# Kernel optimization log

Hardware: AMD Instinct MI355X
Metric: run time of the kernel (lower is better)

## Reference

```python
import jax, jax.numpy as jnp
import numpy as np

HEADS = 2
BN_EPS = 1e-5


def _axial_self_attn(x, Wq, Wkv, Wout, bout):
    # x: (b, s, t, c) -- attend along t (the axial sequence dim)
    b, s, t, c = x.shape
    dh = c // HEADS
    q = (x @ Wq).reshape(b, s, t, HEADS, dh)
    k, v = jnp.split(x @ Wkv, 2, axis=-1)  # matches torch .chunk(2, dim=-1)
    k = k.reshape(b, s, t, HEADS, dh)
    v = v.reshape(b, s, t, HEADS, dh)
    dots = jnp.einsum('bsind,bsjnd->bsnij', q, k) * (dh ** -0.5)
    attn = jax.nn.softmax(dots, axis=-1)
    out = jnp.einsum('bsnij,bsjnd->bsind', attn, v).reshape(b, s, t, c)
    return out @ Wout + bout


def setup_inputs() -> dict:
    key = jax.random.key(0)
    ks = jax.random.split(key, 8)
    B, C, H, W = 8, 128, 256, 256
    E = 2 * C
    sd = 0.05
    return {
        'x': jax.random.normal(ks[0], (B, C, H, W), jnp.float32),
        'Wq_h': jax.random.normal(ks[1], (C, C), jnp.float32) * sd,
        'Wkv_h': jax.random.normal(ks[2], (C, 2 * C), jnp.float32) * sd,
        'Wout_h': jax.random.normal(ks[3], (C, C), jnp.float32) * sd,
        'bout_h': jnp.zeros((C,), jnp.float32),
        'Wq_w': jax.random.normal(ks[4], (C, C), jnp.float32) * sd,
        'Wkv_w': jax.random.normal(ks[5], (C, 2 * C), jnp.float32) * sd,
        'Wout_w': jax.random.normal(ks[6], (C, C), jnp.float32) * sd,
        'bout_w': jnp.zeros((C,), jnp.float32),
        'conv_w': jax.random.normal(ks[7], (E, E), jnp.float32) * sd,  # (in, out); torch conv weight[o,i,0,0].T
        'gamma': jnp.ones((E,), jnp.float32),
        'beta': jnp.zeros((E,), jnp.float32),
    }


def reference(x, Wq_h, Wkv_h, Wout_h, bout_h, Wq_w, Wkv_w, Wout_w, bout_w, conv_w, gamma, beta):
    B, C, H, W = x.shape
    # MaxPool2d(2)
    xp = x.reshape(B, C, H // 2, 2, W // 2, 2).max(axis=(3, 5))  # (B,C,H2,W2)
    xc = jnp.transpose(xp, (0, 2, 3, 1))  # (B,H2,W2,C) channels-last
    # AxialAttention, sum_axial_out=True: height-axis attn + width-axis attn
    a_h = _axial_self_attn(jnp.transpose(xc, (0, 2, 1, 3)), Wq_h, Wkv_h, Wout_h, bout_h)
    a_h = jnp.transpose(a_h, (0, 2, 1, 3))
    a_w = _axial_self_attn(xc, Wq_w, Wkv_w, Wout_w, bout_w)
    a = jax.nn.relu(a_h + a_w)
    # cat((x_attn, x), dim=channel) then conv1x1 -> relu -> BatchNorm (batch stats)
    y = jnp.concatenate([a, xc], axis=-1) @ conv_w  # (B,H2,W2,2C)
    y = jax.nn.relu(y)
    mean = y.mean(axis=(0, 1, 2))
    var = y.var(axis=(0, 1, 2))
    y = (y - mean) * jax.lax.rsqrt(var + BN_EPS) * gamma + beta
    return jnp.transpose(y, (0, 3, 1, 2))  # back to NCHW
```

## Files before the change

### kernel.cpp

```cpp
#include <hip/hip_runtime.h>


typedef short v8s __attribute__((ext_vector_type(8)));
typedef short v4s __attribute__((ext_vector_type(4)));
typedef float v4f __attribute__((ext_vector_type(4)));
typedef float v4flt __attribute__((ext_vector_type(4)));

#define LSA 136
#define LSC 264
#define LSP 130

static __device__ __forceinline__ short f2bf(float f){
  unsigned u = __builtin_bit_cast(unsigned, f);
  u = (u + 0x7FFFu + ((u >> 16) & 1u)) >> 16;
  return (short)u;
}
static __device__ __forceinline__ float bf2f(short s){
  unsigned u = ((unsigned)(unsigned short)s) << 16;
  return __builtin_bit_cast(float, u);
}

__global__ void prep_kernel(const float* __restrict__ Wq_h, const float* __restrict__ Wkv_h,
                            const float* __restrict__ Wout_h, const float* __restrict__ Wq_w,
                            const float* __restrict__ Wkv_w, const float* __restrict__ Wout_w,
                            const float* __restrict__ conv_w, short* __restrict__ wt,
                            float* __restrict__ stats){
  int idx = blockIdx.x * 256 + threadIdx.x;
  if (idx < 8192) stats[idx] = 0.0f;
  const float* src; int K, O, base;
  if      (idx <  16384){ base = 0;      K=128; O=128; src=Wq_h;  }
  else if (idx <  49152){ base = 16384;  K=128; O=256; src=Wkv_h; }
  else if (idx <  65536){ base = 49152;  K=128; O=128; src=Wout_h;}
  else if (idx <  81920){ base = 65536;  K=128; O=128; src=Wq_w;  }
  else if (idx < 114688){ base = 81920;  K=128; O=256; src=Wkv_w; }
  else if (idx < 131072){ base = 114688; K=128; O=128; src=Wout_w;}
  else                  { base = 131072; K=256; O=256; src=conv_w;}
  int local = idx - base;
  int o = local / K, i = local - o * K;
  wt[idx] = f2bf(src[i * O + o]);
}

__global__ __launch_bounds__(256, 4)
void pool_kernel(const float* __restrict__ x, short* __restrict__ xph,
                 short* __restrict__ xpw){
  __shared__ short t_[128*LSP];
  int bx = blockIdx.x;
  int b = bx >> 7, i = bx & 127;
  int tid = (int)threadIdx.x;
  int j2 = tid & 63;
  int cq = tid >> 6;
  for (int rep = 0; rep < 32; ++rep){
    int c = cq*32 + rep;
    const float* p0 = x + (((b*128 + c)*256 + 2*i)*256 + 4*j2);
    v4flt a  = *(const v4flt*)p0;
    v4flt bb = *(const v4flt*)(p0 + 256);
    t_[(2*j2)*LSP + c]   = f2bf(fmaxf(fmaxf(a[0], a[1]), fmaxf(bb[0], bb[1])));
    t_[(2*j2+1)*LSP + c] = f2bf(fmaxf(fmaxf(a[2], a[3]), fmaxf(bb[2], bb[3])));
  }
  __syncthreads();
  int obase_h = ((b*128 + i)*128)*128;
  for (int rep = 0; rep < 8; ++rep){
    int idx = rep*256 + tid;
    int row = idx >> 4, seg = idx & 15;
    v8s v = *(const v8s*)(&t_[row*LSP + seg*8]);
    *(v8s*)(xph + obase_h + row*128 + seg*8) = v;
    *(v8s*)(xpw + ((b*128 + row)*128 + i)*128 + seg*8) = v;
  }
}

__global__ __launch_bounds__(512, 4)
void attn_kernel(const short* __restrict__ xp_hw, const short* __restrict__ xp_wh,
                 const short* __restrict__ wt,
                 const float* __restrict__ bout_h, const float* __restrict__ bout_w,
                 short* __restrict__ ah, short* __restrict__ aw){
  __shared__ short A[128*LSA];
  __shared__ short WB[128*LSA];

  const int bx = blockIdx.x;
  const int dir = bx & 1;
  const int sb = bx >> 1;
  const int b = sb >> 7, s = sb & 127;
  const int tid = (int)threadIdx.x;
  const int w = tid >> 6;
  const int m = w >> 1;
  const int p = w & 1;
  const int lane = tid & 63;
  const int l15 = lane & 15, l4 = lane >> 4;

  const short* Wq   = wt + dir*65536;
  const short* Wk   = Wq + 16384;
  const short* Wv   = Wq + 32768;
  const short* Wout = Wq + 49152;
  const float* bsrc = dir ? bout_w : bout_h;
  const short* xsrc = dir ? xp_hw : xp_wh;
  short*       ao   = dir ? aw : ah;

  v8s av[2][4];
  #pragma unroll
  for (int ti = 0; ti < 2; ++ti){
    int xbase = ((b*128 + s)*128 + (32*m + 16*ti + l15))*128;
    #pragma unroll
    for (int kk = 0; kk < 4; ++kk)
      av[ti][kk] = *(const v8s*)(xsrc + xbase + kk*32 + l4*8);
  }

#define STAGE_W(SRC)                                                     \
  { _Pragma("unroll")                                                    \
    for (int r_ = 0; r_ < 4; ++r_){                                      \
      int idx_ = (r_*512 + tid) * 8;                                     \
      int oc_ = idx_ >> 7, ic_ = idx_ & 127;                             \
      *(v8s*)(&WB[oc_*LSA + ic_]) = *(const v8s*)((SRC) + idx_);         \
    } }

#define WGEMM_TO_A()                                                     \
  { _Pragma("unroll")                                                    \
    for (int ti = 0; ti < 2; ++ti){                                      \
      _Pragma("unroll")                                                  \
      for (int tc = 0; tc < 4; ++tc){                                    \
        int ocb = 64*p + 16*tc;                                          \
        v4f d = {0.f,0.f,0.f,0.f};                                       \
        _Pragma("unroll")                                                \
        for (int kk = 0; kk < 4; ++kk){                                  \
          v8s bf = *(const v8s*)(&WB[(ocb + l15)*LSA + kk*32 + l4*8]);   \
          d = __builtin_amdgcn_mfma_f32_16x16x32_bf16(av[ti][kk], bf, d, 0, 0, 0); \
        }                                                                \
        _Pragma("unroll")                                                \
        for (int r = 0; r < 4; ++r)                                      \
          A[(32*m + 16*ti + 4*l4 + r)*LSA + ocb + l15] = f2bf(d[r]);     \
      } } }

  STAGE_W(Wq);
  __syncthreads();

  WGEMM_TO_A();
  __syncthreads();

  v8s bq[2][2];
  #pragma unroll
  for (int h = 0; h < 2; ++h)
    #pragma unroll
    for (int kk = 0; kk < 2; ++kk)
      bq[h][kk] = *(const v8s*)(&A[(16*w + l15)*LSA + h*64 + kk*32 + l4*8]);
  STAGE_W(Wk);
  __syncthreads();

  WGEMM_TO_A();
  __syncthreads();

  STAGE_W(Wv);

  v4s pk[2][8];
  #pragma unroll
  for (int h = 0; h < 2; ++h){
    v4f st[8];
    #pragma unroll
    for (int jt = 0; jt < 8; ++jt){
      v4f d = {0.f,0.f,0.f,0.f};
      #pragma unroll
      for (int kk = 0; kk < 2; ++kk){
        v8s ak = *(const v8s*)(&A[(16*jt + l15)*LSA + h*64 + kk*32 + l4*8]);
        d = __builtin_amdgcn_mfma_f32_16x16x32_bf16(ak, bq[h][kk], d, 0, 0, 0);
      }
      st[jt] = d;
    }
    float mx = -1e30f;
    #pragma unroll
    for (int jt = 0; jt < 8; ++jt)
      #pragma unroll
      for (int r = 0; r < 4; ++r) mx = fmaxf(mx, st[jt][r]);
    mx = fmaxf(mx, __shfl_xor(mx, 16));
    mx = fmaxf(mx, __shfl_xor(mx, 32));
    float sm = 0.f;
    #pragma unroll
    for (int jt = 0; jt < 8; ++jt)
      #pragma unroll
      for (int r = 0; r < 4; ++r){
        float e = __expf((st[jt][r] - mx) * 0.125f);
        st[jt][r] = e; sm += e;
      }
    sm += __shfl_xor(sm, 16);
    sm += __shfl_xor(sm, 32);
    float inv = 1.0f / sm;
    #pragma unroll
    for (int jt = 0; jt < 8; ++jt)
      #pragma unroll
      for (int r = 0; r < 4; ++r) pk[h][jt][r] = f2bf(st[jt][r] * inv);
  }
  __syncthreads();

  v8s pa[2][4];
  #pragma unroll
  for (int h = 0; h < 2; ++h){
    #pragma unroll
    for (int jt = 0; jt < 8; ++jt)
      *(v4s*)(&A[(16*w + l15)*LSA + 16*jt + 4*l4]) = pk[h][jt];
    #pragma unroll
    for (int kk = 0; kk < 4; ++kk)
      pa[h][kk] = *(const v8s*)(&A[(16*w + l15)*LSA + kk*32 + l4*8]);
  }
  __syncthreads();

  #pragma unroll
  for (int ti = 0; ti < 2; ++ti){
    #pragma unroll
    for (int tc = 0; tc < 4; ++tc){
      int ocb = 64*p + 16*tc;
      v4f d = {0.f,0.f,0.f,0.f};
      #pragma unroll
      for (int kk = 0; kk < 4; ++kk){
        v8s bf = *(const v8s*)(&WB[(ocb + l15)*LSA + kk*32 + l4*8]);
        d = __builtin_amdgcn_mfma_f32_16x16x32_bf16(av[ti][kk], bf, d, 0, 0, 0);
      }
      v4s pkv;
      #pragma unroll
      for (int r = 0; r < 4; ++r) pkv[r] = f2bf(d[r]);
      *(v4s*)(&A[(ocb + l15)*LSA + 32*m + 16*ti + 4*l4]) = pkv;
    }
  }
  __syncthreads();

  STAGE_W(Wout);

  v4f ot[2][4];
  #pragma unroll
  for (int h = 0; h < 2; ++h)
    #pragma unroll
    for (int tc = 0; tc < 4; ++tc){
      v4f d = {0.f,0.f,0.f,0.f};
      #pragma unroll
      for (int kk = 0; kk < 4; ++kk){
        v8s vf = *(const v8s*)(&A[(64*h + 16*tc + l15)*LSA + kk*32 + l4*8]);
        d = __builtin_amdgcn_mfma_f32_16x16x32_bf16(vf, pa[h][kk], d, 0, 0, 0);
      }
      ot[h][tc] = d;
    }
  __syncthreads();

  #pragma unroll
  for (int h = 0; h < 2; ++h)
    #pragma unroll
    for (int tc = 0; tc < 4; ++tc){
      v4s pko;
      #pragma unroll
      for (int r = 0; r < 4; ++r) pko[r] = f2bf(ot[h][tc][r]);
      *(v4s*)(&A[(16*w + l15)*LSA + 64*h + 16*tc + 4*l4]) = pko;
    }
  v8s ob[4];
  #pragma unroll
  for (int kk = 0; kk < 4; ++kk)
    ob[kk] = *(const v8s*)(&A[(16*w + l15)*LSA + kk*32 + l4*8]);
  #pragma unroll
  for (int tc = 0; tc < 8; ++tc){
    v4f d = {0.f,0.f,0.f,0.f};
    #pragma unroll
    for (int kk = 0; kk < 4; ++kk){
      v8s awf = *(const v8s*)(&WB[(tc*16 + l15)*LSA + kk*32 + l4*8]);
      d = __builtin_amdgcn_mfma_f32_16x16x32_bf16(awf, ob[kk], d, 0, 0, 0);
    }
    v4f bias = *(const v4f*)(bsrc + 16*tc + 4*l4);
    v4s z;
    #pragma unroll
    for (int r = 0; r < 4; ++r) z[r] = f2bf(d[r] + bias[r]);
    *(v4s*)(&A[(16*w + l15)*LSA + 16*tc + 4*l4]) = z;
  }
  __syncthreads();

  int obase = ((b*128 + s)*128)*128;
  #pragma unroll
  for (int r = 0; r < 4; ++r){
    int idx = (r*512 + tid) * 8;
    int t = idx >> 7, c = idx & 127;
    *(v8s*)(ao + obase + t*128 + c) = *(const v8s*)(&A[t*LSA + c]);
  }
#undef STAGE_W
#undef WGEMM_TO_A
}

__global__ __launch_bounds__(512, 2)
void conv_kernel(const short* __restrict__ ah, const short* __restrict__ aw,
                 const short* __restrict__ xp, const short* __restrict__ wt,
                 short* __restrict__ yb, float* __restrict__ stats){
  __shared__ short cats[128*LSC];
  __shared__ float lsum[256];
  __shared__ float lsq[256];
  const short* convT = wt + 131072;
  int bx = blockIdx.x;
  int b = bx >> 7, ii = bx & 127;
  int tid = (int)threadIdx.x;
  int wv = tid >> 6, lane = tid & 63, l15 = lane & 15, l4 = lane >> 4;
  if (tid < 256){ lsum[tid] = 0.f; lsq[tid] = 0.f; }

  v8s wf[2][8];
  #pragma unroll
  for (int x = 0; x < 2; ++x)
    #pragma unroll
    for (int kk = 0; kk < 8; ++kk)
      wf[x][kk] = *(const v8s*)(convT + (((wv + 8*x)*16 + l15)*256) + kk*32 + l4*8);

  for (int r = 0; r < 4; ++r){
    int idx = (r*512 + tid) * 8;
    int t = idx >> 7, c = idx & 127;
    v8s hv = *(const v8s*)(ah + ((b*128 + t)*128 + ii)*128 + c);
    v8s wv_ = *(const v8s*)(aw + ((b*128 + ii)*128 + t)*128 + c);
    v8s o;
    #pragma unroll
    for (int k = 0; k < 8; ++k)
      o[k] = f2bf(fmaxf(bf2f(hv[k]) + bf2f(wv_[k]), 0.f));
    *(v8s*)(&cats[t*LSC + c]) = o;
    *(v8s*)(&cats[t*LSC + 128 + c]) =
        *(const v8s*)(xp + ((b*128 + ii)*128 + t)*128 + c);
  }
  __syncthreads();

  v4s ypk[2][8];
  float s1[2] = {0.f,0.f}, s2[2] = {0.f,0.f};
  #pragma unroll
  for (int tt = 0; tt < 8; ++tt){
    v4f d0 = {0.f,0.f,0.f,0.f}, d1 = {0.f,0.f,0.f,0.f};
    #pragma unroll
    for (int kk = 0; kk < 8; ++kk){
      v8s af = *(const v8s*)(&cats[(16*tt + l15)*LSC + kk*32 + l4*8]);
      d0 = __builtin_amdgcn_mfma_f32_16x16x32_bf16(af, wf[0][kk], d0, 0, 0, 0);
      d1 = __builtin_amdgcn_mfma_f32_16x16x32_bf16(af, wf[1][kk], d1, 0, 0, 0);
    }
    #pragma unroll
    for (int r = 0; r < 4; ++r){
      float y0 = fmaxf(d0[r], 0.f), y1 = fmaxf(d1[r], 0.f);
      ypk[0][tt][r] = f2bf(y0); ypk[1][tt][r] = f2bf(y1);
      s1[0] += y0; s2[0] += y0*y0;
      s1[1] += y1; s2[1] += y1*y1;
    }
  }
  #pragma unroll
  for (int x = 0; x < 2; ++x){
    s1[x] += __shfl_xor(s1[x], 16); s1[x] += __shfl_xor(s1[x], 32);
    s2[x] += __shfl_xor(s2[x], 16); s2[x] += __shfl_xor(s2[x], 32);
  }
  if (l4 == 0){
    #pragma unroll
    for (int x = 0; x < 2; ++x){
      int e = (wv + 8*x)*16 + l15;
      atomicAdd(&lsum[e], s1[x]);
      atomicAdd(&lsq[e],  s2[x]);
    }
  }
  __syncthreads();
  #pragma unroll
  for (int x = 0; x < 2; ++x)
    #pragma unroll
    for (int tt = 0; tt < 8; ++tt)
      *(v4s*)(&cats[((wv + 8*x)*16 + l15)*132 + 16*tt + 4*l4]) = ypk[x][tt];
  __syncthreads();
  for (int r = 0; r < 8; ++r){
    int idx = (r*512 + tid) * 8;
    int e = idx >> 7, j = idx & 127;
    *(v8s*)(yb + ((b*256 + e)*128 + ii)*128 + j) = *(const v8s*)(&cats[e*132 + j]);
  }
  if (tid < 256){
    int c = bx & 15;
    atomicAdd(&stats[c*512 + tid],       lsum[tid]);
    atomicAdd(&stats[c*512 + 256 + tid], lsq[tid]);
  }
}

__global__ void bn_kernel(const short* __restrict__ yb, float* __restrict__ out,
                          const float* __restrict__ stats,
                          const float* __restrict__ gamma, const float* __restrict__ beta){
  const float invn = 1.0f / 131072.0f;
  int bx = blockIdx.x;
  int e = bx & 255;
  float s1 = 0.f, s2 = 0.f;
  #pragma unroll
  for (int c = 0; c < 16; ++c){
    s1 += stats[c*512 + e];
    s2 += stats[c*512 + 256 + e];
  }
  float m   = s1 * invn;
  float var = s2 * invn - m * m;
  float sc  = gamma[e] * rsqrtf(var + 1e-5f);
  float sh  = beta[e] - m * sc;
  int base = bx * 16384;
  int tid = (int)threadIdx.x;
  for (int rep = 0; rep < 8; ++rep){
    int idx = base + (rep*256 + tid)*8;
    v8s yv = *(const v8s*)(yb + idx);
    v4f o1, o2;
    #pragma unroll
    for (int r = 0; r < 4; ++r){
      o1[r] = bf2f(yv[r])   * sc + sh;
      o2[r] = bf2f(yv[4+r]) * sc + sh;
    }
    *(v4f*)(out + idx)     = o1;
    *(v4f*)(out + idx + 4) = o2;
  }
}

extern "C" void kernel_launch(void* const* d_in, const int* in_sizes, int n_in,
                              void* d_out, int out_size, void* d_ws, size_t ws_size,
                              hipStream_t stream){
  const float* x      = (const float*)d_in[0];
  const float* Wq_h   = (const float*)d_in[1];
  const float* Wkv_h  = (const float*)d_in[2];
  const float* Wout_h = (const float*)d_in[3];
  const float* bout_h = (const float*)d_in[4];
  const float* Wq_w   = (const float*)d_in[5];
  const float* Wkv_w  = (const float*)d_in[6];
  const float* Wout_w = (const float*)d_in[7];
  const float* bout_w = (const float*)d_in[8];
  const float* conv_w = (const float*)d_in[9];
  const float* gamma  = (const float*)d_in[10];
  const float* beta   = (const float*)d_in[11];
  float* out = (float*)d_out;

  char* ws = (char*)d_ws;
  short* xp_hw = (short*)(ws);
  short* xp_wh = (short*)(ws +  33554432);
  short* ah    = (short*)(ws +  67108864);
  short* aw    = (short*)(ws + 100663296);
  short* yb    = (short*)(ws + 134217728);
  short* wt    = (short*)(ws + 201326592);
  float* stats = (float*)(ws + 201719808);

  prep_kernel<<<768, 256, 0, stream>>>(Wq_h, Wkv_h, Wout_h, Wq_w, Wkv_w, Wout_w,
                                       conv_w, wt, stats);
  pool_kernel<<<1024, 256, 0, stream>>>(x, xp_hw, xp_wh);
  attn_kernel<<<2048, 512, 0, stream>>>(xp_hw, xp_wh, wt, bout_h, bout_w, ah, aw);
  conv_kernel<<<1024, 512, 0, stream>>>(ah, aw, xp_hw, wt, yb, stats);
  bn_kernel<<<2048, 256, 0, stream>>>(yb, out, stats, gamma, beta);
}
```

Before: 304.2 us.

## Process two axial rows per attention block sharing staged weight tiles

The attention kernel now launches 1024-thread blocks that each handle two sequence rows, with one 512-thread half per row. Each half has its own activation buffer in shared memory, while the weight tile is staged into shared memory once and used by both halves. The weight GEMM macro is also restructured to interleave the two row tiles per weight fragment load, and the transposed V write path is folded into the same macro. This halves weight staging traffic and block count, at the cost of more shared memory per block and larger barriers that now synchronise 1024 threads.

```diff
diff --git a/kernel.cpp b/kernel.cpp
--- a/kernel.cpp
+++ b/kernel.cpp
@@ -68,24 +68,29 @@
   }
 }
 
-__global__ __launch_bounds__(512, 4)
+__global__ __launch_bounds__(1024, 4)
 void attn_kernel(const short* __restrict__ xp_hw, const short* __restrict__ xp_wh,
                  const short* __restrict__ wt,
                  const float* __restrict__ bout_h, const float* __restrict__ bout_w,
                  short* __restrict__ ah, short* __restrict__ aw){
-  __shared__ short A[128*LSA];
+  __shared__ short A2[2][128*LSA];
   __shared__ short WB[128*LSA];
 
   const int bx = blockIdx.x;
   const int dir = bx & 1;
   const int sb = bx >> 1;
-  const int b = sb >> 7, s = sb & 127;
+  const int b = sb >> 6, sp = sb & 63;
   const int tid = (int)threadIdx.x;
-  const int w = tid >> 6;
+  const int prob = tid >> 9;
+  const int ptid = tid & 511;
+  const int w = ptid >> 6;
   const int m = w >> 1;
   const int p = w & 1;
   const int lane = tid & 63;
   const int l15 = lane & 15, l4 = lane >> 4;
+  const int s = sp*2 + prob;
+
+  short* A = &A2[prob][0];
 
   const short* Wq   = wt + dir*65536;
   const short* Wk   = Wq + 16384;
@@ -106,33 +111,41 @@
 
 #define STAGE_W(SRC)                                                     \
   { _Pragma("unroll")                                                    \
-    for (int r_ = 0; r_ < 4; ++r_){                                      \
-      int idx_ = (r_*512 + tid) * 8;                                     \
+    for (int r_ = 0; r_ < 2; ++r_){                                      \
+      int idx_ = (r_*1024 + tid) * 8;                                    \
       int oc_ = idx_ >> 7, ic_ = idx_ & 127;                             \
       *(v8s*)(&WB[oc_*LSA + ic_]) = *(const v8s*)((SRC) + idx_);         \
     } }
 
-#define WGEMM_TO_A()                                                     \
+#define WGEMM(TRANS)                                                     \
   { _Pragma("unroll")                                                    \
-    for (int ti = 0; ti < 2; ++ti){                                      \
+    for (int tc = 0; tc < 4; ++tc){                                      \
+      int ocb = 64*p + 16*tc;                                            \
+      v4f d0 = {0.f,0.f,0.f,0.f}, d1 = {0.f,0.f,0.f,0.f};                \
       _Pragma("unroll")                                                  \
-      for (int tc = 0; tc < 4; ++tc){                                    \
-        int ocb = 64*p + 16*tc;                                          \
-        v4f d = {0.f,0.f,0.f,0.f};                                       \
+      for (int kk = 0; kk < 4; ++kk){                                    \
+        v8s bf = *(const v8s*)(&WB[(ocb + l15)*LSA + kk*32 + l4*8]);     \
+        d0 = __builtin_amdgcn_mfma_f32_16x16x32_bf16(av[0][kk], bf, d0, 0, 0, 0); \
+        d1 = __builtin_amdgcn_mfma_f32_16x16x32_bf16(av[1][kk], bf, d1, 0, 0, 0); \
+      }                                                                  \
+      if (TRANS){                                                        \
+        v4s k0, k1;                                                      \
         _Pragma("unroll")                                                \
-        for (int kk = 0; kk < 4; ++kk){                                  \
-          v8s bf = *(const v8s*)(&WB[(ocb + l15)*LSA + kk*32 + l4*8]);   \
-          d = __builtin_amdgcn_mfma_f32_16x16x32_bf16(av[ti][kk], bf, d, 0, 0, 0); \
+        for (int r = 0; r < 4; ++r){ k0[r] = f2bf(d0[r]); k1[r] = f2bf(d1[r]); } \
+        *(v4s*)(&A[(ocb + l15)*LSA + 32*m + 4*l4])      = k0;            \
+        *(v4s*)(&A[(ocb + l15)*LSA + 32*m + 16 + 4*l4]) = k1;            \
+      } else {                                                           \
+        _Pragma("unroll")                                                \
+        for (int r = 0; r < 4; ++r){                                     \
+          A[(32*m + 4*l4 + r)*LSA + ocb + l15]      = f2bf(d0[r]);       \
+          A[(32*m + 16 + 4*l4 + r)*LSA + ocb + l15] = f2bf(d1[r]);       \
         }                                                                \
-        _Pragma("unroll")                                                \
-        for (int r = 0; r < 4; ++r)                                      \
-          A[(32*m + 16*ti + 4*l4 + r)*LSA + ocb + l15] = f2bf(d[r]);     \
       } } }
 
   STAGE_W(Wq);
   __syncthreads();
 
-  WGEMM_TO_A();
+  WGEMM(0);
   __syncthreads();
 
   v8s bq[2][2];
@@ -144,7 +157,7 @@
   STAGE_W(Wk);
   __syncthreads();
 
-  WGEMM_TO_A();
+  WGEMM(0);
   __syncthreads();
 
   STAGE_W(Wv);
@@ -200,23 +213,7 @@
   }
   __syncthreads();
 
-  #pragma unroll
-  for (int ti = 0; ti < 2; ++ti){
-    #pragma unroll
-    for (int tc = 0; tc < 4; ++tc){
-      int ocb = 64*p + 16*tc;
-      v4f d = {0.f,0.f,0.f,0.f};
-      #pragma unroll
-      for (int kk = 0; kk < 4; ++kk){
-        v8s bf = *(const v8s*)(&WB[(ocb + l15)*LSA + kk*32 + l4*8]);
-        d = __builtin_amdgcn_mfma_f32_16x16x32_bf16(av[ti][kk], bf, d, 0, 0, 0);
-      }
-      v4s pkv;
-      #pragma unroll
-      for (int r = 0; r < 4; ++r) pkv[r] = f2bf(d[r]);
-      *(v4s*)(&A[(ocb + l15)*LSA + 32*m + 16*ti + 4*l4]) = pkv;
-    }
-  }
+  WGEMM(1);
   __syncthreads();
 
   STAGE_W(Wout);
@@ -268,12 +265,12 @@
   int obase = ((b*128 + s)*128)*128;
   #pragma unroll
   for (int r = 0; r < 4; ++r){
-    int idx = (r*512 + tid) * 8;
+    int idx = (r*512 + ptid) * 8;
     int t = idx >> 7, c = idx & 127;
     *(v8s*)(ao + obase + t*128 + c) = *(const v8s*)(&A[t*LSA + c]);
   }
 #undef STAGE_W
-#undef WGEMM_TO_A
+#undef WGEMM
 }
 
 __global__ __launch_bounds__(512, 2)
@@ -424,7 +421,7 @@
   prep_kernel<<<768, 256, 0, stream>>>(Wq_h, Wkv_h, Wout_h, Wq_w, Wkv_w, Wout_w,
                                        conv_w, wt, stats);
   pool_kernel<<<1024, 256, 0, stream>>>(x, xp_hw, xp_wh);
-  attn_kernel<<<2048, 512, 0, stream>>>(xp_hw, xp_wh, wt, bout_h, bout_w, ah, aw);
+  attn_kernel<<<1024, 1024, 0, stream>>>(xp_hw, xp_wh, wt, bout_h, bout_w, ah, aw);
   conv_kernel<<<1024, 512, 0, stream>>>(ah, aw, xp_hw, wt, yb, stats);
   bn_kernel<<<2048, 256, 0, stream>>>(yb, out, stats, gamma, beta);
 }
```

Result: faster. 291.2 us (-4.3%).
